# Optimization experiments

Measured on AMD Instinct MI355X. Metric: run time of the kernel, lower is better.

Reference implementation:

```python
import jax, jax.numpy as jnp
import numpy as np

NEG = -1e12  # additive causal mask value used in the original TF code


def setup_inputs() -> dict:
    key = jax.random.key(0)
    k1, k2, k3, k4 = jax.random.split(key, 4)
    B, T, D, U = 4, 4096, 128, 128
    query = jax.random.normal(k1, (B, T, D), dtype=jnp.float32)
    # glorot-style scaled dense weights (no bias, matching use_bias=False)
    s = 1.0 / np.sqrt(D)
    Wq = jax.random.normal(k2, (D, U), dtype=jnp.float32) * s
    Wk = jax.random.normal(k3, (D, U), dtype=jnp.float32) * s
    Wv = jax.random.normal(k4, (D, U), dtype=jnp.float32) * s
    return {"query": query, "Wq": Wq, "Wk": Wk, "Wv": Wv}


def reference(query, Wq, Wk, Wv):
    # Self-attention path: value = key = query (pre-projection)
    q = jnp.einsum('btd,du->btu', query, Wq)
    k = jnp.einsum('btd,du->btu', query, Wk)
    v = jnp.einsum('btd,du->btu', query, Wv)
    T = v.shape[1]
    # NOTE: original scales by sqrt(seq_len) (tf.shape(value)[1]), kept faithfully
    scores = jnp.einsum('bqu,bku->bqk', q, k) / jnp.sqrt(jnp.asarray(T, jnp.float32))
    # additive causal mask: lower-triangular kept, upper gets -1e12
    causal = jnp.tril(jnp.ones((T, T), dtype=jnp.float32))
    scores = scores + NEG * (1.0 - causal)
    attn = jax.nn.softmax(scores, axis=-1)
    context = jnp.einsum('bqk,bku->bqu', attn, v)
    return context
```

## Files before the change

kernel.cpp:

```cpp
#include <hip/hip_runtime.h>

#define T_SEQ 4096
#define BATCH 4
#define DD 128
#define BT (BATCH * T_SEQ)
#define MAXPARTS 4

typedef __bf16 bf16x8 __attribute__((ext_vector_type(8)));
typedef float f32x4 __attribute__((ext_vector_type(4)));

__device__ inline bf16x8 ld8(const unsigned short* p) {
  return *reinterpret_cast<const bf16x8*>(p);
}
__device__ inline unsigned short bfc(float f) {
  __bf16 v = (__bf16)f;
  return __builtin_bit_cast(unsigned short, v);
}
__device__ inline float fexp2(float x) {
  float r;
  asm("v_exp_f32 %0, %1" : "=v"(r) : "v"(x));
  return r;
}
__device__ inline int vsw(int sIdx) {
  return sIdx ^ ((((sIdx >> 6) & 3) << 3));
}

#define MFMA(a, b, c) __builtin_amdgcn_mfma_f32_16x16x32_bf16((a), (b), (c), 0, 0, 0)

__global__ void wt_kernel(const float* __restrict__ Wq, const float* __restrict__ Wk,
                          const float* __restrict__ Wv,
                          unsigned short* __restrict__ fq, unsigned short* __restrict__ fk,
                          unsigned short* __restrict__ fv) {
  const float* W = (blockIdx.y == 0) ? Wq : (blockIdx.y == 1) ? Wk : Wv;
  unsigned short* F = (blockIdx.y == 0) ? fq : (blockIdx.y == 1) ? fk : fv;
  int e = blockIdx.x * 256 + threadIdx.x;
  int j = e & 7, lane = (e >> 3) & 63, nc = e >> 9;
  int c = nc & 3, n0 = nc >> 2;
  int t = lane & 15, g = lane >> 4;
  F[e] = bfc(W[(c * 32 + g * 8 + j) * 128 + n0 * 16 + t]);
}

__global__ __launch_bounds__(256) void proj_kernel(
    const float* __restrict__ X,
    const unsigned short* __restrict__ fq,
    const unsigned short* __restrict__ fk,
    const unsigned short* __restrict__ fv,
    unsigned short* __restrict__ qf,
    unsigned short* __restrict__ kf,
    unsigned short* __restrict__ vt) {
  const int tid = threadIdx.x;
  const int w = tid >> 6, lane = tid & 63;
  const int t = lane & 15, g = lane >> 4;
  const int r0 = blockIdx.x * 32;

  __shared__ unsigned short xs[2][16 * 136];

  bf16x8 wq[2][4], wk[2][4], wv[2][4];
#pragma unroll
  for (int s = 0; s < 2; ++s)
#pragma unroll
    for (int c = 0; c < 4; ++c) {
      int fo = (((w + s * 4) * 4 + c) * 64 + lane) * 8;
      wq[s][c] = ld8(fq + fo);
      wk[s][c] = ld8(fk + fo);
      wv[s][c] = ld8(fv + fo);
    }

#pragma unroll
  for (int sub = 0; sub < 2; ++sub) {
    int r = tid >> 4, cb = tid & 15;
    const float* xp = X + (size_t)(r0 + sub * 16 + r) * DD + cb * 8;
    float4 lo = *reinterpret_cast<const float4*>(xp);
    float4 hi = *reinterpret_cast<const float4*>(xp + 4);
    bf16x8 tmp;
    tmp[0] = (__bf16)lo.x; tmp[1] = (__bf16)lo.y; tmp[2] = (__bf16)lo.z; tmp[3] = (__bf16)lo.w;
    tmp[4] = (__bf16)hi.x; tmp[5] = (__bf16)hi.y; tmp[6] = (__bf16)hi.z; tmp[7] = (__bf16)hi.w;
    *reinterpret_cast<bf16x8*>(&xs[sub][r * 136 + cb * 8]) = tmp;
  }
  __syncthreads();

#pragma unroll
  for (int sub = 0; sub < 2; ++sub) {
    const int r0s = r0 + sub * 16;
    bf16x8 x[4];
#pragma unroll
    for (int c = 0; c < 4; ++c)
      x[c] = ld8(&xs[sub][t * 136 + c * 32 + g * 8]);

#pragma unroll
    for (int s = 0; s < 2; ++s) {
      const int n0 = w + s * 4;
      f32x4 aq = {0.f, 0.f, 0.f, 0.f}, ak = {0.f, 0.f, 0.f, 0.f};
#pragma unroll
      for (int c = 0; c < 4; ++c) {
        aq = MFMA(x[c], wq[s][c], aq);
        ak = MFMA(x[c], wk[s][c], ak);
      }
      const int cP = n0 >> 1;
      const int Gp = ((n0 & 1) << 1) | (t >> 3);
      const int ep = t & 7;
#pragma unroll
      for (int r = 0; r < 4; ++r) {
        int row = r0s + g * 4 + r;
        size_t qoff = ((size_t)((row >> 4) * 4 + cP) * 64 + ((Gp << 4) | (row & 15))) * 8 + ep;
        qf[qoff] = bfc(aq[r] * 0.0225421101f);
        int tp = (row & 3) | (((row >> 3) & 3) << 2);
        size_t koff =
            ((size_t)(((row >> 5) * 2 + ((row >> 2) & 1)) * 4 + cP) * 64 + ((Gp << 4) | tp)) * 8 +
            ep;
        kf[koff] = bfc(ak[r]);
      }
    }

    const int key = r0s + t;
    const size_t vbase = (size_t)(key >> 5) * 4096 + (key & 31);
#pragma unroll
    for (int s = 0; s < 2; ++s) {
      const int u0 = w + s * 4;
      f32x4 av = {0.f, 0.f, 0.f, 0.f};
#pragma unroll
      for (int c = 0; c < 4; ++c)
        av = MFMA(wv[s][c], x[c], av);
#pragma unroll
      for (int r = 0; r < 4; ++r)
        vt[vbase + (size_t)(u0 * 16 + g * 4 + r) * 32] = bfc(av[r]);
    }
  }
}

__global__ __launch_bounds__(256, 2) void attn_kernel(
    const unsigned short* __restrict__ qf,
    const unsigned short* __restrict__ kf,
    const unsigned short* __restrict__ vt,
    float* __restrict__ pO,
    float* __restrict__ pL,
    float* __restrict__ out) {
  const int tid = threadIdx.x;
  const int w = tid >> 6, lane = tid & 63;
  const int t = lane & 15, G = lane >> 4;
  const int bi = blockIdx.x;
  const int xcd = bi & 7;
  const int b = xcd >> 1;
  const int k = ((bi >> 3) << 1) | (xcd & 1);

  const int a = 79 - k;
  int o = 0;
  while (4 * (o + 1) * (o + 2) <= a) ++o;
  const int idx = a - 4 * o * (o + 1);
  const int sg = 8 * o + idx / (o + 1);
  const int p = idx % (o + 1);
  const int parts = o + 1;
  const int N = 4 * sg + 4;
  const int qn = N / parts, rem = N % parts;
  const int jlo = p * qn + min(p, rem);
  const int jhi = jlo + qn + (p < rem ? 1 : 0);

  const int sig32 = 4 * sg + w;
  const int q0 = sig32 * 32;

  const unsigned short* kfb = kf + (size_t)b * (T_SEQ * DD);
  const unsigned short* vtb = vt + (size_t)b * (T_SEQ * DD);

  __shared__ unsigned short bufK[2][4096], bufV[2][4096];

  bf16x8 qa[2][4];
#pragma unroll
  for (int pp = 0; pp < 2; ++pp)
#pragma unroll
    for (int c = 0; c < 4; ++c)
      qa[pp][c] = ld8(qf + ((size_t)((b * 256 + 2 * sig32 + pp) * 4 + c) * 64 + lane) * 8);

  f32x4 O[2][8];
#pragma unroll
  for (int pp = 0; pp < 2; ++pp)
#pragma unroll
    for (int u0 = 0; u0 < 8; ++u0) O[pp][u0] = (f32x4){0.f, 0.f, 0.f, 0.f};
  float ls0 = 0.f, ls1 = 0.f;

  bf16x8 st0, st1, st2, st3;
  {
    const unsigned short* kch = kfb + (size_t)jlo * 4096;
    const unsigned short* vch = vtb + (size_t)jlo * 4096;
    st0 = ld8(kch + tid * 8);
    st1 = ld8(kch + 2048 + tid * 8);
    st2 = ld8(vch + tid * 8);
    st3 = ld8(vch + 2048 + tid * 8);
    *reinterpret_cast<bf16x8*>(&bufK[0][tid * 8]) = st0;
    *reinterpret_cast<bf16x8*>(&bufK[0][2048 + tid * 8]) = st1;
    *reinterpret_cast<bf16x8*>(&bufV[0][vsw(tid * 8)]) = st2;
    *reinterpret_cast<bf16x8*>(&bufV[0][vsw(2048 + tid * 8)]) = st3;
  }
  __syncthreads();

  int cur = 0;
  for (int j = jlo; j < jhi; ++j) {
    const bool more = (j + 1 < jhi);
    if (more) {
      const unsigned short* kch = kfb + (size_t)(j + 1) * 4096;
      const unsigned short* vch = vtb + (size_t)(j + 1) * 4096;
      st0 = ld8(kch + tid * 8);
      st1 = ld8(kch + 2048 + tid * 8);
      st2 = ld8(vch + tid * 8);
      st3 = ld8(vch + 2048 + tid * 8);
    }

    if (j <= sig32) {
      f32x4 s00 = {0.f, 0.f, 0.f, 0.f}, s01 = {0.f, 0.f, 0.f, 0.f};
      f32x4 s10 = {0.f, 0.f, 0.f, 0.f}, s11 = {0.f, 0.f, 0.f, 0.f};
      {
        bf16x8 kc[4];
#pragma unroll
        for (int c = 0; c < 4; ++c) kc[c] = ld8(&bufK[cur][c * 512 + lane * 8]);
#pragma unroll
        for (int c = 0; c < 4; ++c) {
          s00 = MFMA(kc[c], qa[0][c], s00);
          s10 = MFMA(kc[c], qa[1][c], s10);
        }
#pragma unroll
        for (int c = 0; c < 4; ++c) kc[c] = ld8(&bufK[cur][(4 + c) * 512 + lane * 8]);
#pragma unroll
        for (int c = 0; c < 4; ++c) {
          s01 = MFMA(kc[c], qa[0][c], s01);
          s11 = MFMA(kc[c], qa[1][c], s11);
        }
      }

      bf16x8 pb0, pb1;
      if (j < sig32) {
#pragma unroll
        for (int r = 0; r < 4; ++r) {
          float e00 = fexp2(s00[r]), e01 = fexp2(s01[r]);
          float e10 = fexp2(s10[r]), e11 = fexp2(s11[r]);
          ls0 += e00 + e01;
          ls1 += e10 + e11;
          pb0[r] = (__bf16)e00; pb0[r + 4] = (__bf16)e01;
          pb1[r] = (__bf16)e10; pb1[r + 4] = (__bf16)e11;
        }
      } else {
#pragma unroll
        for (int r = 0; r < 4; ++r) {
          int k0 = j * 32 + G * 8 + r;
          float e00 = (k0 <= q0 + t) ? fexp2(s00[r]) : 0.f;
          float e01 = (k0 + 4 <= q0 + t) ? fexp2(s01[r]) : 0.f;
          float e10 = (k0 <= q0 + 16 + t) ? fexp2(s10[r]) : 0.f;
          float e11 = (k0 + 4 <= q0 + 16 + t) ? fexp2(s11[r]) : 0.f;
          ls0 += e00 + e01;
          ls1 += e10 + e11;
          pb0[r] = (__bf16)e00; pb0[r + 4] = (__bf16)e01;
          pb1[r] = (__bf16)e10; pb1[r + 4] = (__bf16)e11;
        }
      }

#pragma unroll
      for (int u0 = 0; u0 < 8; ++u0) {
        bf16x8 vcu = ld8(&bufV[cur][vsw((u0 * 16 + t) * 32 + G * 8)]);
        O[0][u0] = MFMA(pb0, vcu, O[0][u0]);
        O[1][u0] = MFMA(pb1, vcu, O[1][u0]);
      }
    }

    if (more) {
      const int nxt = cur ^ 1;
      *reinterpret_cast<bf16x8*>(&bufK[nxt][tid * 8]) = st0;
      *reinterpret_cast<bf16x8*>(&bufK[nxt][2048 + tid * 8]) = st1;
      *reinterpret_cast<bf16x8*>(&bufV[nxt][vsw(tid * 8)]) = st2;
      *reinterpret_cast<bf16x8*>(&bufV[nxt][vsw(2048 + tid * 8)]) = st3;
      __syncthreads();
      cur ^= 1;
    }
  }

  float r0s = ls0; r0s += __shfl_xor(r0s, 16); r0s += __shfl_xor(r0s, 32);
  float r1s = ls1; r1s += __shfl_xor(r1s, 16); r1s += __shfl_xor(r1s, 32);
  if (parts == 1) {
    float linv0[4], linv1[4];
#pragma unroll
    for (int r = 0; r < 4; ++r) {
      linv0[r] = 1.0f / __shfl(r0s, G * 4 + r);
      linv1[r] = 1.0f / __shfl(r1s, G * 4 + r);
    }
    float* op0 = out + ((size_t)(b * T_SEQ + q0 + G * 4)) * DD + t;
    float* op1 = op0 + (size_t)16 * DD;
#pragma unroll
    for (int u0 = 0; u0 < 8; ++u0) {
#pragma unroll
      for (int r = 0; r < 4; ++r) {
        op0[(size_t)r * DD + u0 * 16] = O[0][u0][r] * linv0[r];
        op1[(size_t)r * DD + u0 * 16] = O[1][u0][r] * linv1[r];
      }
    }
  } else {
    const int slot = (b * 128 + sig32) * MAXPARTS + p;
    if (lane < 16) {
      pL[slot * 32 + lane] = r0s;
      pL[slot * 32 + 16 + lane] = r1s;
    }
    float* pb = pO + (size_t)slot * 4096 + (size_t)(G * 4) * DD + t;
#pragma unroll
    for (int u0 = 0; u0 < 8; ++u0) {
#pragma unroll
      for (int r = 0; r < 4; ++r) {
        pb[(size_t)r * DD + u0 * 16] = O[0][u0][r];
        pb[(size_t)(16 + r) * DD + u0 * 16] = O[1][u0][r];
      }
    }
  }
}

__global__ __launch_bounds__(256) void comb_kernel(const float* __restrict__ pO,
                                                   const float* __restrict__ pL,
                                                   float* __restrict__ out) {
  const int bi = blockIdx.x;
  const int b = bi >> 7, sig32 = bi & 127;
  const int sg = sig32 >> 2;
  const int parts = sg / 8 + 1;
  if (parts == 1) return;
  const int tid = threadIdx.x;
  const int q = tid >> 3, uc = (tid & 7) * 16;
  const int slot0 = (b * 128 + sig32) * MAXPARTS;

  float ls = 0.f;
  for (int p = 0; p < parts; ++p) ls += pL[(slot0 + p) * 32 + q];
  const float linv = 1.0f / ls;

  float4 acc[4] = {{0,0,0,0},{0,0,0,0},{0,0,0,0},{0,0,0,0}};
  for (int p = 0; p < parts; ++p) {
    const float* src = pO + (size_t)(slot0 + p) * 4096 + (size_t)q * DD + uc;
#pragma unroll
    for (int e = 0; e < 4; ++e) {
      float4 v = *reinterpret_cast<const float4*>(src + e * 4);
      acc[e].x += v.x; acc[e].y += v.y; acc[e].z += v.z; acc[e].w += v.w;
    }
  }
  float* dst = out + ((size_t)(b * T_SEQ + sig32 * 32 + q)) * DD + uc;
#pragma unroll
  for (int e = 0; e < 4; ++e) {
    acc[e].x *= linv; acc[e].y *= linv; acc[e].z *= linv; acc[e].w *= linv;
    *reinterpret_cast<float4*>(dst + e * 4) = acc[e];
  }
}

extern "C" void kernel_launch(void* const* d_in, const int* in_sizes, int n_in,
                              void* d_out, int out_size, void* d_ws, size_t ws_size,
                              hipStream_t stream) {
  const float* X  = (const float*)d_in[0];
  const float* Wq = (const float*)d_in[1];
  const float* Wk = (const float*)d_in[2];
  const float* Wv = (const float*)d_in[3];
  float* out = (float*)d_out;

  unsigned short* qf = (unsigned short*)d_ws;
  unsigned short* kf = qf + (size_t)BT * DD;
  unsigned short* vt = kf + (size_t)BT * DD;
  unsigned short* fq = vt + (size_t)BT * DD;
  unsigned short* fk = fq + DD * DD;
  unsigned short* fv = fk + DD * DD;
  float* pO = (float*)(fv + DD * DD);
  float* pL = pO + (size_t)BATCH * 128 * MAXPARTS * 32 * 128;

  dim3 wt_grid(64, 3);
  wt_kernel<<<wt_grid, 256, 0, stream>>>(Wq, Wk, Wv, fq, fk, fv);
  proj_kernel<<<BT / 32, 256, 0, stream>>>(X, fq, fk, fv, qf, kf, vt);
  attn_kernel<<<320, 256, 0, stream>>>(qf, kf, vt, pO, pL, out);
  comb_kernel<<<512, 256, 0, stream>>>(pO, pL, out);
}
```

Measured before the change: 116.3 us.

## Finer split-K work partition, async global-to-LDS loads, MFMA priority hints

```diff
diff --git a/kernel.cpp b/kernel.cpp
--- a/kernel.cpp
+++ b/kernel.cpp
@@ -4,7 +4,7 @@
 #define BATCH 4
 #define DD 128
 #define BT (BATCH * T_SEQ)
-#define MAXPARTS 4
+#define MAXPARTS 16
 
 typedef __bf16 bf16x8 __attribute__((ext_vector_type(8)));
 typedef float f32x4 __attribute__((ext_vector_type(4)));
@@ -23,6 +23,11 @@
 }
 __device__ inline int vsw(int sIdx) {
   return sIdx ^ ((((sIdx >> 6) & 3) << 3));
+}
+__device__ inline void glds16(const unsigned short* g, unsigned short* l) {
+  __builtin_amdgcn_global_load_lds(
+      (const __attribute__((address_space(1))) unsigned int*)(g),
+      (__attribute__((address_space(3))) unsigned int*)(l), 16, 0, 0);
 }
 
 #define MFMA(a, b, c) __builtin_amdgcn_mfma_f32_16x16x32_bf16((a), (b), (c), 0, 0, 0)
@@ -128,7 +133,7 @@
   }
 }
 
-__global__ __launch_bounds__(256, 2) void attn_kernel(
+__global__ __launch_bounds__(256, 3) void attn_kernel(
     const unsigned short* __restrict__ qf,
     const unsigned short* __restrict__ kf,
     const unsigned short* __restrict__ vt,
@@ -143,15 +148,16 @@
   const int b = xcd >> 1;
   const int k = ((bi >> 3) << 1) | (xcd & 1);
 
-  const int a = 79 - k;
-  int o = 0;
-  while (4 * (o + 1) * (o + 2) <= a) ++o;
-  const int idx = a - 4 * o * (o + 1);
-  const int sg = 8 * o + idx / (o + 1);
-  const int p = idx % (o + 1);
-  const int parts = o + 1;
+  const int a = 271 - k;
+  int sg = 0, cacc = 0;
+  for (;;) {
+    const int pg = (sg + 2) >> 1;
+    if (cacc + pg <= a) { cacc += pg; ++sg; } else break;
+  }
+  const int p = a - cacc;
+  const int P = (sg + 2) >> 1;
   const int N = 4 * sg + 4;
-  const int qn = N / parts, rem = N % parts;
+  const int qn = N / P, rem = N % P;
   const int jlo = p * qn + min(p, rem);
   const int jhi = jlo + qn + (p < rem ? 1 : 0);
 
@@ -177,32 +183,21 @@
     for (int u0 = 0; u0 < 8; ++u0) O[pp][u0] = (f32x4){0.f, 0.f, 0.f, 0.f};
   float ls0 = 0.f, ls1 = 0.f;
 
-  bf16x8 st0, st1, st2, st3;
-  {
-    const unsigned short* kch = kfb + (size_t)jlo * 4096;
-    const unsigned short* vch = vtb + (size_t)jlo * 4096;
-    st0 = ld8(kch + tid * 8);
-    st1 = ld8(kch + 2048 + tid * 8);
-    st2 = ld8(vch + tid * 8);
-    st3 = ld8(vch + 2048 + tid * 8);
-    *reinterpret_cast<bf16x8*>(&bufK[0][tid * 8]) = st0;
-    *reinterpret_cast<bf16x8*>(&bufK[0][2048 + tid * 8]) = st1;
-    *reinterpret_cast<bf16x8*>(&bufV[0][vsw(tid * 8)]) = st2;
-    *reinterpret_cast<bf16x8*>(&bufV[0][vsw(2048 + tid * 8)]) = st3;
-  }
+  auto stage = [&](int sel, int jj) {
+    const unsigned short* kch = kfb + (size_t)jj * 4096;
+    const unsigned short* vch = vtb + (size_t)jj * 4096;
+    glds16(kch + tid * 8,             &bufK[sel][tid * 8]);
+    glds16(kch + 2048 + tid * 8,      &bufK[sel][2048 + tid * 8]);
+    glds16(vch + vsw(tid * 8),        &bufV[sel][tid * 8]);
+    glds16(vch + 2048 + vsw(tid * 8), &bufV[sel][2048 + tid * 8]);
+  };
+
+  stage(0, jlo);
   __syncthreads();
 
   int cur = 0;
   for (int j = jlo; j < jhi; ++j) {
-    const bool more = (j + 1 < jhi);
-    if (more) {
-      const unsigned short* kch = kfb + (size_t)(j + 1) * 4096;
-      const unsigned short* vch = vtb + (size_t)(j + 1) * 4096;
-      st0 = ld8(kch + tid * 8);
-      st1 = ld8(kch + 2048 + tid * 8);
-      st2 = ld8(vch + tid * 8);
-      st3 = ld8(vch + 2048 + tid * 8);
-    }
+    if (j + 1 < jhi) stage(cur ^ 1, j + 1);
 
     if (j <= sig32) {
       f32x4 s00 = {0.f, 0.f, 0.f, 0.f}, s01 = {0.f, 0.f, 0.f, 0.f};
@@ -211,18 +206,22 @@
         bf16x8 kc[4];
 #pragma unroll
         for (int c = 0; c < 4; ++c) kc[c] = ld8(&bufK[cur][c * 512 + lane * 8]);
+        __builtin_amdgcn_s_setprio(1);
 #pragma unroll
         for (int c = 0; c < 4; ++c) {
           s00 = MFMA(kc[c], qa[0][c], s00);
           s10 = MFMA(kc[c], qa[1][c], s10);
         }
+        __builtin_amdgcn_s_setprio(0);
 #pragma unroll
         for (int c = 0; c < 4; ++c) kc[c] = ld8(&bufK[cur][(4 + c) * 512 + lane * 8]);
+        __builtin_amdgcn_s_setprio(1);
 #pragma unroll
         for (int c = 0; c < 4; ++c) {
           s01 = MFMA(kc[c], qa[0][c], s01);
           s11 = MFMA(kc[c], qa[1][c], s11);
         }
+        __builtin_amdgcn_s_setprio(0);
       }
 
       bf16x8 pb0, pb1;
@@ -251,28 +250,23 @@
         }
       }
 
+      __builtin_amdgcn_s_setprio(1);
 #pragma unroll
       for (int u0 = 0; u0 < 8; ++u0) {
         bf16x8 vcu = ld8(&bufV[cur][vsw((u0 * 16 + t) * 32 + G * 8)]);
         O[0][u0] = MFMA(pb0, vcu, O[0][u0]);
         O[1][u0] = MFMA(pb1, vcu, O[1][u0]);
       }
-    }
-
-    if (more) {
-      const int nxt = cur ^ 1;
-      *reinterpret_cast<bf16x8*>(&bufK[nxt][tid * 8]) = st0;
-      *reinterpret_cast<bf16x8*>(&bufK[nxt][2048 + tid * 8]) = st1;
-      *reinterpret_cast<bf16x8*>(&bufV[nxt][vsw(tid * 8)]) = st2;
-      *reinterpret_cast<bf16x8*>(&bufV[nxt][vsw(2048 + tid * 8)]) = st3;
-      __syncthreads();
-      cur ^= 1;
-    }
+      __builtin_amdgcn_s_setprio(0);
+    }
+
+    __syncthreads();
+    cur ^= 1;
   }
 
   float r0s = ls0; r0s += __shfl_xor(r0s, 16); r0s += __shfl_xor(r0s, 32);
   float r1s = ls1; r1s += __shfl_xor(r1s, 16); r1s += __shfl_xor(r1s, 32);
-  if (parts == 1) {
+  if (P == 1) {
     float linv0[4], linv1[4];
 #pragma unroll
     for (int r = 0; r < 4; ++r) {
@@ -313,7 +307,7 @@
   const int bi = blockIdx.x;
   const int b = bi >> 7, sig32 = bi & 127;
   const int sg = sig32 >> 2;
-  const int parts = sg / 8 + 1;
+  const int parts = (sg + 2) >> 1;
   if (parts == 1) return;
   const int tid = threadIdx.x;
   const int q = tid >> 3, uc = (tid & 7) * 16;
@@ -361,6 +355,6 @@
   dim3 wt_grid(64, 3);
   wt_kernel<<<wt_grid, 256, 0, stream>>>(Wq, Wk, Wv, fq, fk, fv);
   proj_kernel<<<BT / 32, 256, 0, stream>>>(X, fq, fk, fv, qf, kf, vt);
-  attn_kernel<<<320, 256, 0, stream>>>(qf, kf, vt, pO, pL, out);
+  attn_kernel<<<1088, 256, 0, stream>>>(qf, kf, vt, pO, pL, out);
   comb_kernel<<<512, 256, 0, stream>>>(pO, pL, out);
 }
```

New measurement: 119.0 us. 1.02x slower.
